# Kernel optimization log

Hardware: AMD Instinct MI355X
Metric: run time of the kernel (lower is better)

The kernel has to match this reference:

```python
import jax, jax.numpy as jnp
import numpy as np

R = 3            # corr_radius
KK = 2 * R + 1   # 7
K = KK * KK      # 49 support points
LEVELS = 4       # corr_levels


def _offsets():
    # matches get_support_points: meshgrid over [-r, r] applied to (x, y)
    d = jnp.arange(-R, R + 1, dtype=jnp.float32)
    ox, oy = jnp.meshgrid(d, d, indexing='ij')
    return jnp.stack([ox, oy], -1).reshape(K, 2)


def _bilinear(fmap_flat, fidx, x, y):
    """Bilinear sample with zero padding (grid_sample align_corners=True semantics
    for pixel-space coords). fmap_flat: (F,H,W,D); fidx int (...); x,y float (...).
    Returns (..., D)."""
    Hs, Ws = fmap_flat.shape[1], fmap_flat.shape[2]
    x0 = jnp.floor(x); y0 = jnp.floor(y)
    tx = x - x0; ty = y - y0

    def tap(xi, yi, w):
        valid = (xi >= 0) & (xi <= Ws - 1) & (yi >= 0) & (yi <= Hs - 1)
        xc = jnp.clip(xi, 0, Ws - 1).astype(jnp.int32)
        yc = jnp.clip(yi, 0, Hs - 1).astype(jnp.int32)
        return fmap_flat[fidx, yc, xc] * (w * valid)[..., None]

    return (tap(x0, y0, (1 - tx) * (1 - ty)) + tap(x0 + 1, y0, tx * (1 - ty))
            + tap(x0, y0 + 1, (1 - tx) * ty) + tap(x0 + 1, y0 + 1, tx * ty))


def reference(fmaps, coords, queried_coords, queried_frames, w1, b1, w2, b2):
    """Multi-scale correlation-volume pipeline of CoTrackerThreeOffline:
    L2-normalize fmaps, build avg-pool pyramid, sample 7x7 track-support feats
    at query frames, sample 7x7 correlation feats at current coords per frame,
    einsum 49x49 corr volume, corr_mlp (2401->384 GELU ->256), concat levels."""
    B, T, D, H, W = fmaps.shape
    N = coords.shape[2]
    fm = jnp.transpose(fmaps, (0, 1, 3, 4, 2))  # (B,T,H,W,D)
    fm = fm / jnp.sqrt(jnp.maximum(jnp.sum(fm * fm, -1, keepdims=True), 1e-12))
    offs = _offsets()
    fidx_t = jnp.arange(B * T).reshape(B, T, 1, 1)          # frame index per (b,t)
    fq = (jnp.arange(B)[:, None] * T + queried_frames)[..., None]  # (B,N,1)
    embs = []
    for lvl in range(LEVELS):
        Hs, Ws = fm.shape[2], fm.shape[3]
        fm_flat = fm.reshape(B * T, Hs, Ws, D)
        # track support features at the query frame (7x7 around query coord)
        qc = queried_coords / (2.0 ** lvl)                   # (B,N,2)
        px = qc[..., 0:1] + offs[:, 0]; py = qc[..., 1:2] + offs[:, 1]  # (B,N,K)
        tf = _bilinear(fm_flat, fq, px, py)                  # (B,N,K,D)
        # correlation features around current coords for every frame
        cl = coords / (2.0 ** lvl)                           # (B,T,N,2)
        cx = cl[..., 0:1] + offs[:, 0]; cy = cl[..., 1:2] + offs[:, 1]  # (B,T,N,K)
        cf = _bilinear(fm_flat, fidx_t, cx, cy)              # (B,T,N,K,D)
        # 49x49 correlation volume then corr_mlp
        vol = jnp.einsum('btnkc,bnlc->btnkl', cf, tf).reshape(B * T * N, K * K)
        emb = jax.nn.gelu(vol @ w1 + b1, approximate=False) @ w2 + b2
        embs.append(emb.reshape(B, T, N, -1))
        if lvl < LEVELS - 1:  # avg_pool2d k=2 s=2
            fm = fm.reshape(B, T, Hs // 2, 2, Ws // 2, 2, D).mean(axis=(3, 5))
    return jnp.concatenate(embs, -1)  # (B,T,N,4*256)


def setup_inputs() -> dict:
    key = jax.random.key(0)
    ks = jax.random.split(key, 6)
    B, T, D, H, W, N = 1, 24, 128, 96, 128, 256
    fmaps = jax.random.normal(ks[0], (B, T, D, H, W), jnp.float32)
    scale_xy = jnp.array([W - 1.0, H - 1.0], jnp.float32)
    queried_coords = jax.random.uniform(ks[1], (B, N, 2), jnp.float32) * scale_xy
    queried_frames = jax.random.randint(ks[2], (B, N), 0, T)
    coords = jax.random.uniform(ks[3], (B, T, N, 2), jnp.float32) * scale_xy
    w1 = jax.random.normal(ks[4], (K * K, 384), jnp.float32) * 0.02
    b1 = jnp.zeros((384,), jnp.float32)
    w2 = jax.random.normal(ks[5], (384, 256), jnp.float32) * 0.02
    b2 = jnp.zeros((256,), jnp.float32)
    return dict(fmaps=fmaps, coords=coords, queried_coords=queried_coords,
                queried_frames=queried_frames, w1=w1, b1=b1, w2=w2, b2=b2)
```

## Files before the change

kernel.cpp:

```cpp
#include <hip/hip_runtime.h>
#include <hip/hip_bf16.h>
#include <stdint.h>

#define T_   24
#define D_   128
#define H_   96
#define W_   128
#define N_   256
#define KP   49
#define K2   3136
#define H1   384
#define OUTC 256
#define MTOT (4 * T_ * N_)

#define PAD  8

typedef __attribute__((ext_vector_type(8))) __bf16 bf16x8;
typedef __attribute__((ext_vector_type(4))) float f32x4;

typedef __attribute__((address_space(3))) unsigned int lds_u32;
typedef const __attribute__((address_space(1))) unsigned int g_u32;
#define GLOAD16(g, l) __builtin_amdgcn_global_load_lds((g_u32*)(g), (lds_u32*)(l), 16, 0, 0)

__device__ inline float bf2f(unsigned short u) {
    union { unsigned int i; float f; } v; v.i = ((unsigned int)u) << 16; return v.f;
}
__device__ inline unsigned short f2bf(float f) {
    union { float f; unsigned int i; } v; v.f = f;
    unsigned int i = v.i;
    return (unsigned short)((i + 0x7FFFu + ((i >> 16) & 1u)) >> 16);
}

__global__ __launch_bounds__(256) void k_padzero(uint4* __restrict__ fm,
                                                 int Hs, int Ws) {
    int PW = Ws + 2 * PAD, PH = Hs + 2 * PAD;
    size_t upf = (size_t)PH * PW * 16;
    size_t total = upf * T_;
    for (size_t idx = (size_t)blockIdx.x * 256 + threadIdx.x; idx < total;
         idx += (size_t)gridDim.x * 256) {
        size_t p = idx >> 4;
        size_t pf = p % ((size_t)PH * PW);
        int y = (int)(pf / PW), x = (int)(pf % PW);
        if (y < PAD || y >= Hs + PAD || x < PAD || x >= Ws + PAD) {
            uint4 z = {0u, 0u, 0u, 0u};
            fm[idx] = z;
        }
    }
}

__global__ __launch_bounds__(256) void k_w1t(const float* __restrict__ w1,
                                             unsigned short* __restrict__ w1t) {
    int idx = blockIdx.x * 256 + threadIdx.x;
    if (idx >= H1 * K2) return;
    int nn = idx / K2, kk = idx % K2;
    int k = kk >> 6, l = kk & 63;
    float v = (l < KP) ? w1[((size_t)k * KP + l) * H1 + nn] : 0.f;
    w1t[idx] = f2bf(v);
}
__global__ __launch_bounds__(256) void k_w2t(const float* __restrict__ w2,
                                             unsigned short* __restrict__ w2t) {
    int idx = blockIdx.x * 256 + threadIdx.x;
    if (idx >= OUTC * H1) return;
    int j = idx / H1, k = idx % H1;
    w2t[idx] = f2bf(w2[(size_t)k * OUTC + j]);
}

#define PW0 (W_ + 2 * PAD)
#define FR0 ((size_t)(H_ + 2 * PAD) * PW0 * D_)
__global__ __launch_bounds__(256) void k_normalize(const float* __restrict__ fmaps,
                                                   unsigned short* __restrict__ fm0i) {
    int bid = blockIdx.x;
    int t = bid / H_, h = bid % H_;
    int tid = threadIdx.x;
    __shared__ float tile[64 * 129];
    __shared__ float ssumP[64][4];
    __shared__ float rs[64];
    const float* base = fmaps + (size_t)t * D_ * H_ * W_ + (size_t)h * W_;
    unsigned short* orow = fm0i + (size_t)t * FR0 + (size_t)h * (PW0 * D_);
    for (int wt = 0; wt < 2; ++wt) {
        int wl = tid & 63, dg = tid >> 6;
        float ss = 0.f;
        for (int i = 0; i < 32; ++i) {
            int d = dg * 32 + i;
            float v = base[(size_t)d * (H_ * W_) + wt * 64 + wl];
            tile[wl * 129 + d] = v;
            ss += v * v;
        }
        ssumP[wl][dg] = ss;
        __syncthreads();
        if (tid < 64)
            rs[tid] = rsqrtf(fmaxf(ssumP[tid][0] + ssumP[tid][1] + ssumP[tid][2] + ssumP[tid][3], 1e-12f));
        __syncthreads();
        int c = tid & 63, rg = tid >> 6;
        for (int i = 0; i < 16; ++i) {
            int wll = rg * 16 + i;
            float r = rs[wll];
            float v0 = tile[wll * 129 + c * 2] * r;
            float v1 = tile[wll * 129 + c * 2 + 1] * r;
            *(unsigned int*)(orow + (size_t)(wt * 64 + wll) * D_ + c * 2) =
                (unsigned int)f2bf(v0) | ((unsigned int)f2bf(v1) << 16);
        }
        __syncthreads();
    }
}

__global__ __launch_bounds__(256) void k_pool(const unsigned short* __restrict__ ini,
                                              unsigned short* __restrict__ outi,
                                              int Hs, int Ws) {
    int Ho = Hs >> 1, Wo = Ws >> 1;
    int PWi = Ws + 2 * PAD, PWo = Wo + 2 * PAD;
    size_t FRi = (size_t)(Hs + 2 * PAD) * PWi * D_;
    size_t FRo = (size_t)(Ho + 2 * PAD) * PWo * D_;
    size_t total = (size_t)T_ * Ho * Wo * (D_ / 4);
    size_t idx = (size_t)blockIdx.x * 256 + threadIdx.x;
    if (idx >= total) return;
    int d4 = idx & 31;
    size_t p = idx >> 5;
    int x = (int)(p % Wo); p /= Wo;
    int y = (int)(p % Ho); int t = (int)(p / Ho);
    const unsigned short* b0 = ini + (size_t)t * FRi + ((size_t)(2 * y) * PWi + 2 * x) * D_ + d4 * 4;
    const unsigned short* b1r = b0 + (size_t)PWi * D_;
    float acc[4] = {0.f, 0.f, 0.f, 0.f};
#pragma unroll
    for (int j = 0; j < 2; ++j) {
        const unsigned short* bb = j ? b1r : b0;
#pragma unroll
        for (int i = 0; i < 2; ++i) {
            const unsigned short* q = bb + i * D_;
#pragma unroll
            for (int c = 0; c < 4; ++c) acc[c] += bf2f(q[c]);
        }
    }
    unsigned short* o = outi + (size_t)t * FRo + ((size_t)y * PWo + x) * D_ + d4 * 4;
#pragma unroll
    for (int c = 0; c < 4; ++c) o[c] = f2bf(acc[c] * 0.25f);
}

__device__ inline float2 bilin2p(const unsigned short* __restrict__ fb, int PW,
                                 float px, float py, int lane) {
    float x0f = floorf(px), y0f = floorf(py);
    float tx = px - x0f, ty = py - y0f;
    int x0 = (int)x0f, y0 = (int)y0f;
    float acc0 = 0.f, acc1 = 0.f;
#pragma unroll
    for (int dy = 0; dy < 2; ++dy) {
#pragma unroll
        for (int dx = 0; dx < 2; ++dx) {
            long xi = x0 + dx, yi = y0 + dy;
            float w = (dx ? tx : 1.f - tx) * (dy ? ty : 1.f - ty);
            unsigned int pk = *(const unsigned int*)(fb + (yi * PW + xi) * D_ + lane * 2);
            acc0 += w * bf2f((unsigned short)(pk & 0xffffu));
            acc1 += w * bf2f((unsigned short)(pk >> 16));
        }
    }
    return {acc0, acc1};
}

__global__ __launch_bounds__(256) void k_tf(const unsigned short* __restrict__ f0,
                                            const unsigned short* __restrict__ f1,
                                            const unsigned short* __restrict__ f2,
                                            const unsigned short* __restrict__ f3,
                                            const float* __restrict__ qcoords,
                                            const int* __restrict__ qframes,
                                            unsigned short* __restrict__ tfg) {
    int n = blockIdx.x, lvl = blockIdx.y;
    const unsigned short* fmi = lvl == 0 ? f0 : lvl == 1 ? f1 : lvl == 2 ? f2 : f3;
    int Hs = H_ >> lvl, Ws = W_ >> lvl;
    int PW = Ws + 2 * PAD;
    size_t FR = (size_t)(Hs + 2 * PAD) * PW * D_;
    float inv = 1.0f / (float)(1 << lvl);
    int wid = threadIdx.x >> 6, lane = threadIdx.x & 63;
    int fidx = qframes[n];
    float qx = qcoords[n * 2 + 0] * inv, qy = qcoords[n * 2 + 1] * inv;
    const unsigned short* fb = fmi + (size_t)fidx * FR;
    unsigned short* orow = tfg + ((size_t)lvl * N_ + n) * (64 * D_);
    for (int k = wid; k < 64; k += 4) {
        float2 v = {0.f, 0.f};
        if (k < KP) {
            float px = qx + (float)(k / 7 - 3);
            float py = qy + (float)(k % 7 - 3);
            v = bilin2p(fb, PW, px, py, lane);
        }
        unsigned int pk = (unsigned int)f2bf(v.x) | ((unsigned int)f2bf(v.y) << 16);
        *(unsigned int*)(orow + k * D_ + lane * 2) = pk;
    }
}

__global__ __launch_bounds__(256) void k_cfvol(const unsigned short* __restrict__ f0,
                                               const unsigned short* __restrict__ f1,
                                               const unsigned short* __restrict__ f2,
                                               const unsigned short* __restrict__ f3,
                                               const float* __restrict__ coords,
                                               const unsigned short* __restrict__ tfg,
                                               unsigned short* __restrict__ vol) {
    __shared__ unsigned char tfs[16384];
    __shared__ unsigned char Ps[16384];
    __shared__ unsigned short Gs[64 * 64];
    int n = blockIdx.x, t = blockIdx.y, lvl = blockIdx.z;
    const unsigned short* fmi = lvl == 0 ? f0 : lvl == 1 ? f1 : lvl == 2 ? f2 : f3;
    int Hs = H_ >> lvl, Ws = W_ >> lvl;
    int PW = Ws + 2 * PAD;
    size_t FR = (size_t)(Hs + 2 * PAD) * PW * D_;
    float inv = 1.0f / (float)(1 << lvl);
    int tid = threadIdx.x, wid = tid >> 6, lane = tid & 63;
    int l15 = lane & 15, hi = lane >> 4;

    float cx = coords[((size_t)t * N_ + n) * 2 + 0] * inv;
    float cy = coords[((size_t)t * N_ + n) * 2 + 1] * inv;
    float fx = floorf(cx), fy = floorf(cy);
    float tx = cx - fx, ty = cy - fy;
    long bx = (long)(int)fx - 3, by = (long)(int)fy - 3;
    const unsigned short* fb = fmi + (size_t)t * FR;
    const unsigned short* tfn = tfg + ((size_t)lvl * N_ + n) * (64 * D_);
#pragma unroll
    for (int i = 0; i < 4; ++i) {
        int rr = wid * 16 + i * 4 + hi;
        int u = l15 ^ (rr & 7);
        GLOAD16(tfn + rr * 128 + u * 8, tfs + (wid * 4 + i) * 1024);
    }
#pragma unroll
    for (int i = 0; i < 4; ++i) {
        int rr = wid * 16 + i * 4 + hi;
        int u = l15 ^ (rr & 7);
        GLOAD16(fb + ((by + (rr & 7)) * (long)PW + (bx + (rr >> 3))) * D_ + u * 8,
                Ps + (wid * 4 + i) * 1024);
    }
    asm volatile("s_waitcnt vmcnt(0)" ::: "memory");
    __builtin_amdgcn_s_barrier();
    f32x4 acc[4] = {f32x4{0,0,0,0}, f32x4{0,0,0,0}, f32x4{0,0,0,0}, f32x4{0,0,0,0}};
#pragma unroll
    for (int ks = 0; ks < 4; ++ks) {
        int colb = ks * 64 + hi * 16;
        int arow = wid * 16 + l15;
        bf16x8 a = *(const bf16x8*)(Ps + arow * 256 + (colb ^ ((arow & 7) << 4)));
#pragma unroll
        for (int ln = 0; ln < 4; ++ln) {
            int brow = ln * 16 + l15;
            bf16x8 b = *(const bf16x8*)(tfs + brow * 256 + (colb ^ ((brow & 7) << 4)));
            acc[ln] = __builtin_amdgcn_mfma_f32_16x16x32_bf16(a, b, acc[ln], 0, 0, 0);
        }
    }
#pragma unroll
    for (int ln = 0; ln < 4; ++ln)
#pragma unroll
        for (int r = 0; r < 4; ++r)
            Gs[(wid * 16 + hi * 4 + r) * 64 + ln * 16 + l15] = f2bf(acc[ln][r]);
    __syncthreads();
    unsigned int* vrow = (unsigned int*)(vol + (((size_t)lvl * T_ + t) * N_ + n) * K2);
    float w00 = (1.f - tx) * (1.f - ty), w01 = (1.f - tx) * ty;
    float w10 = tx * (1.f - ty), w11 = tx * ty;
    int lh = lane >> 5, ll = lane & 31;
#pragma unroll
    for (int it = 0; it < 7; ++it) {
        int k = it * 8 + wid * 2 + lh;
        if (k < KP) {
            int a0 = k / 7, b0 = k - a0 * 7;
            int g = a0 * 8 + b0;
            const unsigned short* gp = &Gs[g * 64 + ll * 2];
            unsigned int u00 = *(const unsigned int*)(gp);
            unsigned int u01 = *(const unsigned int*)(gp + 64);
            unsigned int u10 = *(const unsigned int*)(gp + 8 * 64);
            unsigned int u11 = *(const unsigned int*)(gp + 9 * 64);
            float r0 = w00 * bf2f((unsigned short)u00) + w01 * bf2f((unsigned short)u01)
                     + w10 * bf2f((unsigned short)u10) + w11 * bf2f((unsigned short)u11);
            float r1 = w00 * bf2f((unsigned short)(u00 >> 16)) + w01 * bf2f((unsigned short)(u01 >> 16))
                     + w10 * bf2f((unsigned short)(u10 >> 16)) + w11 * bf2f((unsigned short)(u11 >> 16));
            vrow[k * 32 + ll] = (unsigned int)f2bf(r0) | ((unsigned int)f2bf(r1) << 16);
        }
    }
}

__global__ __launch_bounds__(256) void k_gemm1(const unsigned short* __restrict__ A,
                                               const unsigned short* __restrict__ Bt,
                                               const float* __restrict__ b1,
                                               unsigned short* __restrict__ Hout) {
    __shared__ unsigned char As[8192];
    __shared__ unsigned char Bs[16384];
    int bid = blockIdx.x;
    int swz = (bid & 7) * 144 + (bid >> 3);
    int bm = swz / 3, bn = swz % 3;
    int tid = threadIdx.x, lane = tid & 63;
    int wid = tid >> 6, wm = wid & 1, wn = wid >> 1;
    int l15 = lane & 15, hi = lane >> 4;
    f32x4 acc[2][4] = {};
    const unsigned short* Abase = A + (size_t)(bm * 64) * K2;
    const unsigned short* Bbase = Bt + (size_t)(bn * 128) * K2;
    for (int kt = 0; kt < K2 / 64; ++kt) {
#pragma unroll
        for (int q = 0; q < 2; ++q) {
            int e = (wid * 2 + q) * 64 + lane;
            int row = e >> 3, su = (e & 7) ^ (row & 7);
            GLOAD16(Abase + (size_t)row * K2 + kt * 64 + su * 8, As + (wid * 2 + q) * 1024);
        }
#pragma unroll
        for (int q = 0; q < 4; ++q) {
            int e = (wid * 4 + q) * 64 + lane;
            int row = e >> 3, su = (e & 7) ^ (row & 7);
            GLOAD16(Bbase + (size_t)row * K2 + kt * 64 + su * 8, Bs + (wid * 4 + q) * 1024);
        }
        __syncthreads();
#pragma unroll
        for (int ks = 0; ks < 2; ++ks) {
            int colb = ks * 64 + hi * 16;
            bf16x8 a[2], b[4];
#pragma unroll
            for (int km = 0; km < 2; ++km) {
                int arow = wm * 32 + km * 16 + l15;
                a[km] = *(const bf16x8*)(As + arow * 128 + (colb ^ ((arow & 7) << 4)));
            }
#pragma unroll
            for (int ln = 0; ln < 4; ++ln) {
                int brow = wn * 64 + ln * 16 + l15;
                b[ln] = *(const bf16x8*)(Bs + brow * 128 + (colb ^ ((brow & 7) << 4)));
            }
#pragma unroll
            for (int km = 0; km < 2; ++km)
#pragma unroll
                for (int ln = 0; ln < 4; ++ln)
                    acc[km][ln] = __builtin_amdgcn_mfma_f32_16x16x32_bf16(a[km], b[ln], acc[km][ln], 0, 0, 0);
        }
        __syncthreads();
    }
#pragma unroll
    for (int km = 0; km < 2; ++km)
#pragma unroll
        for (int ln = 0; ln < 4; ++ln)
#pragma unroll
            for (int r = 0; r < 4; ++r) {
                int row = bm * 64 + wm * 32 + km * 16 + hi * 4 + r;
                int col = bn * 128 + wn * 64 + ln * 16 + l15;
                float x = acc[km][ln][r] + b1[col];
                float g = 0.5f * x * (1.f + erff(x * 0.70710678118654752f));
                Hout[(size_t)row * H1 + col] = f2bf(g);
            }
}

__global__ __launch_bounds__(256) void k_gemm2(const unsigned short* __restrict__ A,
                                               const unsigned short* __restrict__ Bt,
                                               const float* __restrict__ b2,
                                               float* __restrict__ outp) {
    __shared__ unsigned char As[8192];
    __shared__ unsigned char Bs[16384];
    int bid = blockIdx.x;
    int swz = (bid & 7) * 96 + (bid >> 3);
    int bm = swz >> 1, bn = swz & 1;
    int tid = threadIdx.x, lane = tid & 63;
    int wid = tid >> 6, wm = wid & 1, wn = wid >> 1;
    int l15 = lane & 15, hi = lane >> 4;
    f32x4 acc[2][4] = {};
    const unsigned short* Abase = A + (size_t)(bm * 64) * H1;
    const unsigned short* Bbase = Bt + (size_t)(bn * 128) * H1;
    for (int kt = 0; kt < H1 / 64; ++kt) {
#pragma unroll
        for (int q = 0; q < 2; ++q) {
            int e = (wid * 2 + q) * 64 + lane;
            int row = e >> 3, su = (e & 7) ^ (row & 7);
            GLOAD16(Abase + (size_t)row * H1 + kt * 64 + su * 8, As + (wid * 2 + q) * 1024);
        }
#pragma unroll
        for (int q = 0; q < 4; ++q) {
            int e = (wid * 4 + q) * 64 + lane;
            int row = e >> 3, su = (e & 7) ^ (row & 7);
            GLOAD16(Bbase + (size_t)row * H1 + kt * 64 + su * 8, Bs + (wid * 4 + q) * 1024);
        }
        __syncthreads();
#pragma unroll
        for (int ks = 0; ks < 2; ++ks) {
            int colb = ks * 64 + hi * 16;
            bf16x8 a[2], b[4];
#pragma unroll
            for (int km = 0; km < 2; ++km) {
                int arow = wm * 32 + km * 16 + l15;
                a[km] = *(const bf16x8*)(As + arow * 128 + (colb ^ ((arow & 7) << 4)));
            }
#pragma unroll
            for (int ln = 0; ln < 4; ++ln) {
                int brow = wn * 64 + ln * 16 + l15;
                b[ln] = *(const bf16x8*)(Bs + brow * 128 + (colb ^ ((brow & 7) << 4)));
            }
#pragma unroll
            for (int km = 0; km < 2; ++km)
#pragma unroll
                for (int ln = 0; ln < 4; ++ln)
                    acc[km][ln] = __builtin_amdgcn_mfma_f32_16x16x32_bf16(a[km], b[ln], acc[km][ln], 0, 0, 0);
        }
        __syncthreads();
    }
#pragma unroll
    for (int km = 0; km < 2; ++km)
#pragma unroll
        for (int ln = 0; ln < 4; ++ln)
#pragma unroll
            for (int r = 0; r < 4; ++r) {
                int row = bm * 64 + wm * 32 + km * 16 + hi * 4 + r;
                int col = bn * 128 + wn * 64 + ln * 16 + l15;
                int lvl = row / (T_ * N_);
                int r2 = row - lvl * (T_ * N_);
                outp[(size_t)r2 * (4 * OUTC) + lvl * OUTC + col] = acc[km][ln][r] + b2[col];
            }
}

extern "C" void kernel_launch(void* const* d_in, const int* in_sizes, int n_in,
                              void* d_out, int out_size, void* d_ws, size_t ws_size,
                              hipStream_t stream) {
    const float* fmaps   = (const float*)d_in[0];
    const float* coords  = (const float*)d_in[1];
    const float* qcoords = (const float*)d_in[2];
    const int*   qframes = (const int*)d_in[3];
    const float* w1      = (const float*)d_in[4];
    const float* b1      = (const float*)d_in[5];
    const float* w2      = (const float*)d_in[6];
    const float* b2      = (const float*)d_in[7];
    float* outp = (float*)d_out;

    unsigned char* ws = (unsigned char*)d_ws;
    size_t off = 0;
    auto take = [&](size_t bytes) {
        unsigned char* p = ws + off;
        off += (bytes + 255) & ~(size_t)255;
        return p;
    };
    const int Hs[4] = {96, 48, 24, 12}, Wss[4] = {128, 64, 32, 16};
    unsigned short* fmraw[4];
    unsigned short* fmint[4];
    for (int l = 0; l < 4; ++l) {
        int PH = Hs[l] + 2 * PAD, PW = Wss[l] + 2 * PAD;
        fmraw[l] = (unsigned short*)take((size_t)T_ * PH * PW * D_ * 2);
        fmint[l] = fmraw[l] + ((size_t)PAD * PW + PAD) * D_;
    }
    unsigned short* tfg  = (unsigned short*)take((size_t)4 * N_ * 64 * D_ * 2);
    unsigned short* vol  = (unsigned short*)take((size_t)MTOT * K2 * 2);
    unsigned short* hbuf = (unsigned short*)take((size_t)MTOT * H1 * 2);
    unsigned short* w1t  = (unsigned short*)take((size_t)H1 * K2 * 2);
    unsigned short* w2t  = (unsigned short*)take((size_t)OUTC * H1 * 2);

    for (int l = 0; l < 4; ++l)
        hipLaunchKernelGGL(k_padzero, dim3(4096), dim3(256), 0, stream,
                           (uint4*)fmraw[l], Hs[l], Wss[l]);
    hipLaunchKernelGGL(k_w1t, dim3((H1 * K2 + 255) / 256), dim3(256), 0, stream, w1, w1t);
    hipLaunchKernelGGL(k_w2t, dim3((OUTC * H1 + 255) / 256), dim3(256), 0, stream, w2, w2t);
    hipLaunchKernelGGL(k_normalize, dim3(T_ * H_), dim3(256), 0, stream, fmaps, fmint[0]);
    hipLaunchKernelGGL(k_pool, dim3((T_ * 48 * 64 * 32 + 255) / 256), dim3(256), 0, stream,
                       fmint[0], fmint[1], 96, 128);
    hipLaunchKernelGGL(k_pool, dim3((T_ * 24 * 32 * 32 + 255) / 256), dim3(256), 0, stream,
                       fmint[1], fmint[2], 48, 64);
    hipLaunchKernelGGL(k_pool, dim3((T_ * 12 * 16 * 32 + 255) / 256), dim3(256), 0, stream,
                       fmint[2], fmint[3], 24, 32);

    hipLaunchKernelGGL(k_tf, dim3(N_, 4), dim3(256), 0, stream,
                       fmint[0], fmint[1], fmint[2], fmint[3], qcoords, qframes, tfg);
    hipLaunchKernelGGL(k_cfvol, dim3(N_, T_, 4), dim3(256), 0, stream,
                       fmint[0], fmint[1], fmint[2], fmint[3], coords, tfg, vol);
    hipLaunchKernelGGL(k_gemm1, dim3(384 * 3), dim3(256), 0, stream, vol, w1t, b1, hbuf);
    hipLaunchKernelGGL(k_gemm2, dim3(384 * 2), dim3(256), 0, stream, hbuf, w2t, b2, outp);
}
```

Measured before the change: 323.1 us.

## Load track features directly into registers and double GEMM1 K-tile depth

In the correlation-volume kernel, track-support features are now read straight from global memory into MFMA B-operand registers instead of being staged through shared memory. This frees 16 KB of LDS per block and removes a round of LDS reads. The first MLP GEMM now consumes 128-wide K tiles, which halves the number of barrier-separated iterations but doubles its LDS footprint. To make K divisible by 128, K2 is padded from 3136 to 3200: the volume kernel zero-fills the extra columns and the w1 transpose zeroes the padded rows, which adds a little redundant GEMM work.

```diff
diff --git a/kernel.cpp b/kernel.cpp
--- a/kernel.cpp
+++ b/kernel.cpp
@@ -8,7 +8,7 @@
 #define W_   128
 #define N_   256
 #define KP   49
-#define K2   3136
+#define K2   3200
 #define H1   384
 #define OUTC 256
 #define MTOT (4 * T_ * N_)
@@ -54,7 +54,7 @@
     if (idx >= H1 * K2) return;
     int nn = idx / K2, kk = idx % K2;
     int k = kk >> 6, l = kk & 63;
-    float v = (l < KP) ? w1[((size_t)k * KP + l) * H1 + nn] : 0.f;
+    float v = (k < KP && l < KP) ? w1[((size_t)k * KP + l) * H1 + nn] : 0.f;
     w1t[idx] = f2bf(v);
 }
 __global__ __launch_bounds__(256) void k_w2t(const float* __restrict__ w2,
@@ -193,7 +193,6 @@
                                                const float* __restrict__ coords,
                                                const unsigned short* __restrict__ tfg,
                                                unsigned short* __restrict__ vol) {
-    __shared__ unsigned char tfs[16384];
     __shared__ unsigned char Ps[16384];
     __shared__ unsigned short Gs[64 * 64];
     int n = blockIdx.x, t = blockIdx.y, lvl = blockIdx.z;
@@ -216,17 +215,18 @@
     for (int i = 0; i < 4; ++i) {
         int rr = wid * 16 + i * 4 + hi;
         int u = l15 ^ (rr & 7);
-        GLOAD16(tfn + rr * 128 + u * 8, tfs + (wid * 4 + i) * 1024);
-    }
-#pragma unroll
-    for (int i = 0; i < 4; ++i) {
-        int rr = wid * 16 + i * 4 + hi;
-        int u = l15 ^ (rr & 7);
         GLOAD16(fb + ((by + (rr & 7)) * (long)PW + (bx + (rr >> 3))) * D_ + u * 8,
                 Ps + (wid * 4 + i) * 1024);
     }
+    bf16x8 bfr[4][4];
+#pragma unroll
+    for (int ln = 0; ln < 4; ++ln)
+#pragma unroll
+        for (int ks = 0; ks < 4; ++ks)
+            bfr[ln][ks] = *(const bf16x8*)(tfn + (ln * 16 + l15) * 128 + ks * 32 + hi * 8);
     asm volatile("s_waitcnt vmcnt(0)" ::: "memory");
     __builtin_amdgcn_s_barrier();
+    __builtin_amdgcn_sched_barrier(0);
     f32x4 acc[4] = {f32x4{0,0,0,0}, f32x4{0,0,0,0}, f32x4{0,0,0,0}, f32x4{0,0,0,0}};
 #pragma unroll
     for (int ks = 0; ks < 4; ++ks) {
@@ -234,11 +234,8 @@
         int arow = wid * 16 + l15;
         bf16x8 a = *(const bf16x8*)(Ps + arow * 256 + (colb ^ ((arow & 7) << 4)));
 #pragma unroll
-        for (int ln = 0; ln < 4; ++ln) {
-            int brow = ln * 16 + l15;
-            bf16x8 b = *(const bf16x8*)(tfs + brow * 256 + (colb ^ ((brow & 7) << 4)));
-            acc[ln] = __builtin_amdgcn_mfma_f32_16x16x32_bf16(a, b, acc[ln], 0, 0, 0);
-        }
+        for (int ln = 0; ln < 4; ++ln)
+            acc[ln] = __builtin_amdgcn_mfma_f32_16x16x32_bf16(a, bfr[ln][ks], acc[ln], 0, 0, 0);
     }
 #pragma unroll
     for (int ln = 0; ln < 4; ++ln)
@@ -268,14 +265,15 @@
             vrow[k * 32 + ll] = (unsigned int)f2bf(r0) | ((unsigned int)f2bf(r1) << 16);
         }
     }
+    if (tid < 32) vrow[1568 + tid] = 0u;
 }
 
 __global__ __launch_bounds__(256) void k_gemm1(const unsigned short* __restrict__ A,
                                                const unsigned short* __restrict__ Bt,
                                                const float* __restrict__ b1,
                                                unsigned short* __restrict__ Hout) {
-    __shared__ unsigned char As[8192];
-    __shared__ unsigned char Bs[16384];
+    __shared__ unsigned char As[16384];
+    __shared__ unsigned char Bs[32768];
     int bid = blockIdx.x;
     int swz = (bid & 7) * 144 + (bid >> 3);
     int bm = swz / 3, bn = swz % 3;
@@ -285,33 +283,35 @@
     f32x4 acc[2][4] = {};
     const unsigned short* Abase = A + (size_t)(bm * 64) * K2;
     const unsigned short* Bbase = Bt + (size_t)(bn * 128) * K2;
-    for (int kt = 0; kt < K2 / 64; ++kt) {
-#pragma unroll
-        for (int q = 0; q < 2; ++q) {
-            int e = (wid * 2 + q) * 64 + lane;
-            int row = e >> 3, su = (e & 7) ^ (row & 7);
-            GLOAD16(Abase + (size_t)row * K2 + kt * 64 + su * 8, As + (wid * 2 + q) * 1024);
-        }
+    for (int kt = 0; kt < K2 / 128; ++kt) {
 #pragma unroll
         for (int q = 0; q < 4; ++q) {
-            int e = (wid * 4 + q) * 64 + lane;
-            int row = e >> 3, su = (e & 7) ^ (row & 7);
-            GLOAD16(Bbase + (size_t)row * K2 + kt * 64 + su * 8, Bs + (wid * 4 + q) * 1024);
-        }
-        __syncthreads();
-#pragma unroll
-        for (int ks = 0; ks < 2; ++ks) {
+            int e = q * 256 + tid;
+            int row = e >> 4, su = (e & 15) ^ (row & 7);
+            GLOAD16(Abase + (size_t)row * K2 + kt * 128 + su * 8,
+                    As + q * 4096 + wid * 1024);
+        }
+#pragma unroll
+        for (int q = 0; q < 8; ++q) {
+            int e = q * 256 + tid;
+            int row = e >> 4, su = (e & 15) ^ (row & 7);
+            GLOAD16(Bbase + (size_t)row * K2 + kt * 128 + su * 8,
+                    Bs + q * 4096 + wid * 1024);
+        }
+        __syncthreads();
+#pragma unroll
+        for (int ks = 0; ks < 4; ++ks) {
             int colb = ks * 64 + hi * 16;
             bf16x8 a[2], b[4];
 #pragma unroll
             for (int km = 0; km < 2; ++km) {
                 int arow = wm * 32 + km * 16 + l15;
-                a[km] = *(const bf16x8*)(As + arow * 128 + (colb ^ ((arow & 7) << 4)));
+                a[km] = *(const bf16x8*)(As + arow * 256 + (colb ^ ((arow & 7) << 4)));
             }
 #pragma unroll
             for (int ln = 0; ln < 4; ++ln) {
                 int brow = wn * 64 + ln * 16 + l15;
-                b[ln] = *(const bf16x8*)(Bs + brow * 128 + (colb ^ ((brow & 7) << 4)));
+                b[ln] = *(const bf16x8*)(Bs + brow * 256 + (colb ^ ((brow & 7) << 4)));
             }
 #pragma unroll
             for (int km = 0; km < 2; ++km)
```

New measurement: 414.8 us. +28.4%, slower.

## Double-buffer LDS tiles in gemm1 to overlap global loads with MFMA

Applied to the files above, without the earlier changes.

The first GEMM kernel now keeps two LDS buffers for the A and B tiles. It issues the global-to-LDS loads for the next K tile before computing on the current one, and uses explicit vmcnt waits with raw barriers in place of __syncthreads. The goal is to hide global memory latency behind MFMA work. In exchange it doubles LDS use per block, which may lower occupancy, and it depends on the hand-counted vmcnt value being correct.

```diff
diff --git a/kernel.cpp b/kernel.cpp
--- a/kernel.cpp
+++ b/kernel.cpp
@@ -274,8 +274,8 @@
                                                const unsigned short* __restrict__ Bt,
                                                const float* __restrict__ b1,
                                                unsigned short* __restrict__ Hout) {
-    __shared__ unsigned char As[8192];
-    __shared__ unsigned char Bs[16384];
+    __shared__ unsigned char As[2][8192];
+    __shared__ unsigned char Bs[2][16384];
     int bid = blockIdx.x;
     int swz = (bid & 7) * 144 + (bid >> 3);
     int bm = swz / 3, bn = swz % 3;
@@ -285,20 +285,32 @@
     f32x4 acc[2][4] = {};
     const unsigned short* Abase = A + (size_t)(bm * 64) * K2;
     const unsigned short* Bbase = Bt + (size_t)(bn * 128) * K2;
-    for (int kt = 0; kt < K2 / 64; ++kt) {
+    auto STAGE = [&](int kt, int buf) {
 #pragma unroll
         for (int q = 0; q < 2; ++q) {
             int e = (wid * 2 + q) * 64 + lane;
             int row = e >> 3, su = (e & 7) ^ (row & 7);
-            GLOAD16(Abase + (size_t)row * K2 + kt * 64 + su * 8, As + (wid * 2 + q) * 1024);
+            GLOAD16(Abase + (size_t)row * K2 + kt * 64 + su * 8, As[buf] + (wid * 2 + q) * 1024);
         }
 #pragma unroll
         for (int q = 0; q < 4; ++q) {
             int e = (wid * 4 + q) * 64 + lane;
             int row = e >> 3, su = (e & 7) ^ (row & 7);
-            GLOAD16(Bbase + (size_t)row * K2 + kt * 64 + su * 8, Bs + (wid * 4 + q) * 1024);
-        }
-        __syncthreads();
+            GLOAD16(Bbase + (size_t)row * K2 + kt * 64 + su * 8, Bs[buf] + (wid * 4 + q) * 1024);
+        }
+    };
+    const int KT = K2 / 64;
+    STAGE(0, 0);
+    for (int kt = 0; kt < KT; ++kt) {
+        int cur = kt & 1;
+        if (kt + 1 < KT) {
+            STAGE(kt + 1, cur ^ 1);
+            asm volatile("s_waitcnt vmcnt(6)" ::: "memory");
+        } else {
+            asm volatile("s_waitcnt vmcnt(0)" ::: "memory");
+        }
+        __builtin_amdgcn_s_barrier();
+        __builtin_amdgcn_sched_barrier(0);
 #pragma unroll
         for (int ks = 0; ks < 2; ++ks) {
             int colb = ks * 64 + hi * 16;
@@ -306,12 +318,12 @@
 #pragma unroll
             for (int km = 0; km < 2; ++km) {
                 int arow = wm * 32 + km * 16 + l15;
-                a[km] = *(const bf16x8*)(As + arow * 128 + (colb ^ ((arow & 7) << 4)));
+                a[km] = *(const bf16x8*)(As[cur] + arow * 128 + (colb ^ ((arow & 7) << 4)));
             }
 #pragma unroll
             for (int ln = 0; ln < 4; ++ln) {
                 int brow = wn * 64 + ln * 16 + l15;
-                b[ln] = *(const bf16x8*)(Bs + brow * 128 + (colb ^ ((brow & 7) << 4)));
+                b[ln] = *(const bf16x8*)(Bs[cur] + brow * 128 + (colb ^ ((brow & 7) << 4)));
             }
 #pragma unroll
             for (int km = 0; km < 2; ++km)
@@ -319,7 +331,10 @@
                 for (int ln = 0; ln < 4; ++ln)
                     acc[km][ln] = __builtin_amdgcn_mfma_f32_16x16x32_bf16(a[km], b[ln], acc[km][ln], 0, 0, 0);
         }
-        __syncthreads();
+        if (kt + 1 < KT) {
+            __builtin_amdgcn_sched_barrier(0);
+            __builtin_amdgcn_s_barrier();
+        }
     }
 #pragma unroll
     for (int km = 0; km < 2; ++km)
```

Result: slower. 332.6 us (+2.9%).
